# Optimization experiments

Hardware: AMD Instinct MI355X
Metric: run time of the kernel (lower is better)

## Reference

```python
import jax, jax.numpy as jnp
import numpy as np

NUM_EXPERTS = 16
TOP_K = 2
D_STATE = 32
INPUT_DIM = 512
COPIES = 4
B, H, W = 64, 32, 32
NOISE_KEY = jax.random.key(42)


def setup_inputs() -> dict:
    key = jax.random.key(0)
    k1, k2, k3 = jax.random.split(key, 3)
    inputs = jax.random.normal(k1, (B, INPUT_DIM, H, W), dtype=jnp.float32)
    W_route = jax.random.normal(k2, (INPUT_DIM, NUM_EXPERTS), dtype=jnp.float32) * 0.02
    b_route = jnp.zeros((NUM_EXPERTS,), dtype=jnp.float32)
    W_noise = jax.random.normal(k3, (INPUT_DIM, NUM_EXPERTS), dtype=jnp.float32) * 0.02
    b_noise = jnp.zeros((NUM_EXPERTS,), dtype=jnp.float32)
    # A_log_init: log(arange(1..d_state)) repeated over d_inner, copies, merged
    A = jnp.log(jnp.arange(1, D_STATE + 1, dtype=jnp.float32))            # [n]
    A = jnp.broadcast_to(A, (COPIES * INPUT_DIM, D_STATE))                # [copies*d, n]
    A_logs = jnp.broadcast_to(A, (NUM_EXPERTS, COPIES * INPUT_DIM, D_STATE)).copy()
    return {"inputs": inputs, "W_route": W_route, "b_route": b_route,
            "W_noise": W_noise, "b_noise": b_noise, "A_logs": A_logs}


def reference(inputs, W_route, b_route, W_noise, b_noise, A_logs):
    # Router: spatial mean pool -> [B, input_dim]
    x = inputs.mean(axis=(2, 3))
    logits = jax.nn.softmax(x @ W_route + b_route, axis=-1)               # [B, E]
    noise_logits = x @ W_noise + b_noise                                  # [B, E]
    eps = jax.random.normal(NOISE_KEY, logits.shape, dtype=logits.dtype)
    noise = jax.nn.softmax(eps * jax.nn.softplus(noise_logits), axis=-1)
    noisy_logits = logits + noise                                         # [B, E]
    top_k_logits, indices = jax.lax.top_k(noisy_logits, TOP_K)            # [B, k]
    router_output = jax.nn.softmax(top_k_logits, axis=-1)                 # [B, k]
    # Dispatch: gather selected expert A_log tables -> [B, k, copies*d, n]
    expert_outputs = A_logs[indices]
    # Weighted combine then mean over batch -> [copies*d, n]
    combined = jnp.einsum('bnik,bn->bik', expert_outputs, router_output).mean(axis=0)
    # z-loss over noisy logits
    z_loss = jnp.sum(jax.nn.logsumexp(noisy_logits, axis=-1) ** 2) / noisy_logits.shape[0]
    return combined, z_loss
```

## Files before the change

kernel.cpp:

```cpp
#include <hip/hip_runtime.h>
#include <hip/hip_bf16.h>
#include <math.h>
#include <stdint.h>


__global__ __launch_bounds__(256) void k_meanpool(const float* __restrict__ in,
                                                  float* __restrict__ x) {
  int gwave = (blockIdx.x * 256 + threadIdx.x) >> 6;
  int lane  = threadIdx.x & 63;
  const float4* p = reinterpret_cast<const float4*>(in) + (size_t)gwave * 256;
  float s = 0.f;
#pragma unroll
  for (int j = 0; j < 4; ++j) {
    float4 v = p[lane + 64 * j];
    s += (v.x + v.y) + (v.z + v.w);
  }
#pragma unroll
  for (int off = 32; off > 0; off >>= 1) s += __shfl_down(s, off, 64);
  if (lane == 0) x[gwave] = s * (1.0f / 1024.0f);
}

__device__ __forceinline__ uint32_t rotl32(uint32_t v, int d) {
  return (v << d) | (v >> (32 - d));
}

__device__ __forceinline__ void threefry2x32_0_42(uint32_t& x0, uint32_t& x1) {
  const uint32_t k0 = 0u, k1 = 42u;
  const uint32_t ks2 = k0 ^ k1 ^ 0x1BD11BDAu;
  x0 += k0; x1 += k1;
#define RND(rot) { x0 += x1; x1 = rotl32(x1, rot); x1 ^= x0; }
#define G4(a,b,c,d, ka,kb,inc) { RND(a) RND(b) RND(c) RND(d) x0 += ka; x1 += kb + inc; }
  G4(13,15,26,6,  k1,  ks2, 1u)
  G4(17,29,16,24, ks2, k0,  2u)
  G4(13,15,26,6,  k0,  k1,  3u)
  G4(17,29,16,24, k1,  ks2, 4u)
  G4(13,15,26,6,  ks2, k0,  5u)
#undef G4
#undef RND
}

__device__ __forceinline__ float erfinv_f32(float x) {
  float w = -log1pf(-x * x);
  float p;
  if (w < 5.0f) {
    w -= 2.5f;
    p = 2.81022636e-08f;
    p = fmaf(p, w, 3.43273939e-07f);
    p = fmaf(p, w, -3.5233877e-06f);
    p = fmaf(p, w, -4.39150654e-06f);
    p = fmaf(p, w, 0.00021858087f);
    p = fmaf(p, w, -0.00125372503f);
    p = fmaf(p, w, -0.00417768164f);
    p = fmaf(p, w, 0.246640727f);
    p = fmaf(p, w, 1.50140941f);
  } else {
    w = sqrtf(w) - 3.0f;
    p = -0.000200214257f;
    p = fmaf(p, w, 0.000100950558f);
    p = fmaf(p, w, 0.00134934322f);
    p = fmaf(p, w, -0.00367342844f);
    p = fmaf(p, w, 0.00573950773f);
    p = fmaf(p, w, -0.0076224613f);
    p = fmaf(p, w, 0.00943887047f);
    p = fmaf(p, w, 1.00167406f);
    p = fmaf(p, w, 2.83297682f);
  }
  return p * x;
}

__global__ __launch_bounds__(256) void k_router(
    const float* __restrict__ x,
    const float* __restrict__ Wr, const float* __restrict__ br,
    const float* __restrict__ Wn, const float* __restrict__ bn,
    int* __restrict__ idx, float* __restrict__ rw, float* __restrict__ lseArr) {
  __shared__ float xs[512];
  __shared__ float pr[16][17], pn[16][17];
  __shared__ float lg[16], nl[16], npre[16], noisy[16];
  const int b = blockIdx.x, tid = threadIdx.x;

  for (int d = tid; d < 512; d += 256) xs[d] = x[b * 512 + d];
  __syncthreads();

  const int e = tid & 15, c = tid >> 4;
  float sr = 0.f, sn = 0.f;
#pragma unroll 8
  for (int j = 0; j < 32; ++j) {
    int d = c * 32 + j;
    float xv = xs[d];
    sr = fmaf(xv, Wr[d * 16 + e], sr);
    sn = fmaf(xv, Wn[d * 16 + e], sn);
  }
  pr[c][e] = sr;
  pn[c][e] = sn;
  __syncthreads();

  if (tid < 16) {
    float a = 0.f, bb = 0.f;
    for (int cc = 0; cc < 16; ++cc) { a += pr[cc][tid]; bb += pn[cc][tid]; }
    lg[tid] = a + br[tid];
    float v = bb + bn[tid];
    nl[tid] = v;
    uint32_t i  = (uint32_t)(b * 16 + tid);
    uint32_t j  = i & 511u;
    uint32_t x0 = j, x1 = j + 512u;
    threefry2x32_0_42(x0, x1);
    uint32_t bits = (i < 512u) ? x0 : x1;
    float u01 = __uint_as_float((bits >> 9) | 0x3f800000u) - 1.0f;
    const float lo = -0.99999994f;
    float u = fmaf(u01, 1.0f - lo, lo);
    u = fmaxf(lo, u);
    float eps = 1.41421356f * erfinv_f32(u);
    float sp = fmaxf(v, 0.f) + log1pf(expf(-fabsf(v)));
    npre[tid] = eps * sp;
  }
  __syncthreads();

  if (tid < 16) {
    float ml = -INFINITY, mn = -INFINITY;
    for (int q = 0; q < 16; ++q) { ml = fmaxf(ml, lg[q]); mn = fmaxf(mn, npre[q]); }
    float sl = 0.f, sn2 = 0.f;
    for (int q = 0; q < 16; ++q) { sl += expf(lg[q] - ml); sn2 += expf(npre[q] - mn); }
    noisy[tid] = expf(lg[tid] - ml) / sl + expf(npre[tid] - mn) / sn2;
  }
  __syncthreads();

  if (tid == 0) {
    int i0 = 0; float v0 = noisy[0];
    for (int q = 1; q < 16; ++q) if (noisy[q] > v0) { v0 = noisy[q]; i0 = q; }
    int i1 = -1; float v1 = -INFINITY;
    for (int q = 0; q < 16; ++q) {
      if (q == i0) continue;
      if (noisy[q] > v1) { v1 = noisy[q]; i1 = q; }
    }
    float t = expf(v1 - v0);
    float inv = 1.0f / (1.0f + t);
    idx[b * 2 + 0] = i0; idx[b * 2 + 1] = i1;
    rw [b * 2 + 0] = inv; rw [b * 2 + 1] = t * inv;
    float m = -INFINITY;
    for (int q = 0; q < 16; ++q) m = fmaxf(m, noisy[q]);
    float s2 = 0.f;
    for (int q = 0; q < 16; ++q) s2 += expf(noisy[q] - m);
    lseArr[b] = m + logf(s2);
  }
}

__global__ __launch_bounds__(64) void k_reduce(const int* __restrict__ idx,
                                               const float* __restrict__ rw,
                                               const float* __restrict__ lse,
                                               float* __restrict__ w,
                                               float* __restrict__ zout) {
  int tid = threadIdx.x;
  if (tid < 16) {
    float acc = 0.f;
    for (int j = 0; j < 128; ++j)
      if (idx[j] == tid) acc += rw[j];
    w[tid] = acc * (1.0f / 64.0f);
  }
  if (tid == 32) {
    float z = 0.f;
    for (int b = 0; b < 64; ++b) { float l = lse[b]; z += l * l; }
    zout[0] = z * (1.0f / 64.0f);
  }
}

__global__ __launch_bounds__(256) void k_combine(const float* __restrict__ A,
                                                 const float* __restrict__ w,
                                                 float* __restrict__ out) {
  int t = blockIdx.x * 256 + threadIdx.x;
  const float4* A4 = reinterpret_cast<const float4*>(A);
  float4 acc = make_float4(0.f, 0.f, 0.f, 0.f);
#pragma unroll
  for (int e = 0; e < 16; ++e) {
    float we = w[e];
    float4 v = A4[e * 16384 + t];
    acc.x = fmaf(we, v.x, acc.x);
    acc.y = fmaf(we, v.y, acc.y);
    acc.z = fmaf(we, v.z, acc.z);
    acc.w = fmaf(we, v.w, acc.w);
  }
  reinterpret_cast<float4*>(out)[t] = acc;
}

extern "C" void kernel_launch(void* const* d_in, const int* in_sizes, int n_in,
                              void* d_out, int out_size, void* d_ws, size_t ws_size,
                              hipStream_t stream) {
  const float* inputs = (const float*)d_in[0];
  const float* Wr     = (const float*)d_in[1];
  const float* br     = (const float*)d_in[2];
  const float* Wn     = (const float*)d_in[3];
  const float* bn     = (const float*)d_in[4];
  const float* A      = (const float*)d_in[5];
  float* out = (float*)d_out;

  char* ws   = (char*)d_ws;
  float* x   = (float*)(ws);
  int*   idx = (int*)  (ws + 131072);
  float* rw  = (float*)(ws + 131584);
  float* lse = (float*)(ws + 132096);
  float* w   = (float*)(ws + 132352);

  hipLaunchKernelGGL(k_meanpool, dim3(8192), dim3(256), 0, stream, inputs, x);
  hipLaunchKernelGGL(k_router,   dim3(64),   dim3(256), 0, stream, x, Wr, br, Wn, bn, idx, rw, lse);
  hipLaunchKernelGGL(k_reduce,   dim3(1),    dim3(64),  0, stream, idx, rw, lse, w, out + 65536);
  hipLaunchKernelGGL(k_combine,  dim3(64),   dim3(256), 0, stream, A, w, out);
}
```

Baseline: 226.6 us.

## Fuse router, reduce and combine into one kernel with grid-level flag sync

Merges the router, expert-weight reduction and combine kernels into a single 64-block kernel. The last block to arrive, identified through an atomic ticket counter, computes the expert weights and z-loss, then releases a flag that the other blocks spin on before they run the combine. The counter and flag are reset inside the mean-pool kernel, and the mean-pool input reads become nontemporal loads. This removes two kernel launches and their gaps, in exchange for a spin-wait that relies on all 64 blocks being resident at the same time.

```diff
diff --git a/kernel.cpp b/kernel.cpp
--- a/kernel.cpp
+++ b/kernel.cpp
@@ -4,15 +4,22 @@
 #include <stdint.h>
 
 
+#define AGENT __HIP_MEMORY_SCOPE_AGENT
+
+typedef float fvec4 __attribute__((ext_vector_type(4)));
+
 __global__ __launch_bounds__(256) void k_meanpool(const float* __restrict__ in,
-                                                  float* __restrict__ x) {
+                                                  float* __restrict__ x,
+                                                  unsigned int* __restrict__ counter,
+                                                  unsigned int* __restrict__ flag) {
+  if (blockIdx.x == 0 && threadIdx.x == 0) { *counter = 0u; *flag = 0u; }
   int gwave = (blockIdx.x * 256 + threadIdx.x) >> 6;
   int lane  = threadIdx.x & 63;
-  const float4* p = reinterpret_cast<const float4*>(in) + (size_t)gwave * 256;
+  const fvec4* p = reinterpret_cast<const fvec4*>(in) + (size_t)gwave * 256;
   float s = 0.f;
 #pragma unroll
   for (int j = 0; j < 4; ++j) {
-    float4 v = p[lane + 64 * j];
+    fvec4 v = __builtin_nontemporal_load(&p[lane + 64 * j]);
     s += (v.x + v.y) + (v.z + v.w);
   }
 #pragma unroll
@@ -68,14 +75,19 @@
   return p * x;
 }
 
-__global__ __launch_bounds__(256) void k_router(
+__global__ __launch_bounds__(256) void k_tail(
     const float* __restrict__ x,
     const float* __restrict__ Wr, const float* __restrict__ br,
     const float* __restrict__ Wn, const float* __restrict__ bn,
-    int* __restrict__ idx, float* __restrict__ rw, float* __restrict__ lseArr) {
+    const float* __restrict__ A,
+    float* __restrict__ out,
+    int* __restrict__ idx, float* __restrict__ rw, float* __restrict__ lseArr,
+    float* __restrict__ w,
+    unsigned int* __restrict__ counter, unsigned int* __restrict__ flag) {
   __shared__ float xs[512];
   __shared__ float pr[16][17], pn[16][17];
-  __shared__ float lg[16], nl[16], npre[16], noisy[16];
+  __shared__ float lg[16], npre[16], noisy[16];
+  __shared__ unsigned int sTicket;
   const int b = blockIdx.x, tid = threadIdx.x;
 
   for (int d = tid; d < 512; d += 256) xs[d] = x[b * 512 + d];
@@ -99,7 +111,6 @@
     for (int cc = 0; cc < 16; ++cc) { a += pr[cc][tid]; bb += pn[cc][tid]; }
     lg[tid] = a + br[tid];
     float v = bb + bn[tid];
-    nl[tid] = v;
     uint32_t i  = (uint32_t)(b * 16 + tid);
     uint32_t j  = i & 511u;
     uint32_t x0 = j, x1 = j + 512u;
@@ -134,45 +145,63 @@
     }
     float t = expf(v1 - v0);
     float inv = 1.0f / (1.0f + t);
-    idx[b * 2 + 0] = i0; idx[b * 2 + 1] = i1;
-    rw [b * 2 + 0] = inv; rw [b * 2 + 1] = t * inv;
+    __hip_atomic_store(&idx[b * 2 + 0], i0,      __ATOMIC_RELAXED, AGENT);
+    __hip_atomic_store(&idx[b * 2 + 1], i1,      __ATOMIC_RELAXED, AGENT);
+    __hip_atomic_store(&rw [b * 2 + 0], inv,     __ATOMIC_RELAXED, AGENT);
+    __hip_atomic_store(&rw [b * 2 + 1], t * inv, __ATOMIC_RELAXED, AGENT);
     float m = -INFINITY;
     for (int q = 0; q < 16; ++q) m = fmaxf(m, noisy[q]);
     float s2 = 0.f;
     for (int q = 0; q < 16; ++q) s2 += expf(noisy[q] - m);
-    lseArr[b] = m + logf(s2);
-  }
-}
-
-__global__ __launch_bounds__(64) void k_reduce(const int* __restrict__ idx,
-                                               const float* __restrict__ rw,
-                                               const float* __restrict__ lse,
-                                               float* __restrict__ w,
-                                               float* __restrict__ zout) {
-  int tid = threadIdx.x;
-  if (tid < 16) {
-    float acc = 0.f;
-    for (int j = 0; j < 128; ++j)
-      if (idx[j] == tid) acc += rw[j];
-    w[tid] = acc * (1.0f / 64.0f);
-  }
-  if (tid == 32) {
-    float z = 0.f;
-    for (int b = 0; b < 64; ++b) { float l = lse[b]; z += l * l; }
-    zout[0] = z * (1.0f / 64.0f);
-  }
-}
-
-__global__ __launch_bounds__(256) void k_combine(const float* __restrict__ A,
-                                                 const float* __restrict__ w,
-                                                 float* __restrict__ out) {
-  int t = blockIdx.x * 256 + threadIdx.x;
+    __hip_atomic_store(&lseArr[b], m + logf(s2), __ATOMIC_RELAXED, AGENT);
+    __threadfence();
+    sTicket = atomicAdd(counter, 1u);
+  }
+  __syncthreads();
+
+  if (sTicket == 63u) {
+    __threadfence();
+    if (tid < 16) {
+      float acc = 0.f;
+      for (int j = 0; j < 128; ++j) {
+        int ij = __hip_atomic_load(&idx[j], __ATOMIC_RELAXED, AGENT);
+        if (ij == tid) acc += __hip_atomic_load(&rw[j], __ATOMIC_RELAXED, AGENT);
+      }
+      __hip_atomic_store(&w[tid], acc * (1.0f / 64.0f), __ATOMIC_RELAXED, AGENT);
+    }
+    if (tid == 32) {
+      float z = 0.f;
+      for (int bb = 0; bb < 64; ++bb) {
+        float l = __hip_atomic_load(&lseArr[bb], __ATOMIC_RELAXED, AGENT);
+        z += l * l;
+      }
+      out[65536] = z * (1.0f / 64.0f);
+    }
+    __syncthreads();
+    if (tid == 0) {
+      __threadfence();
+      __hip_atomic_store(flag, 1u, __ATOMIC_RELEASE, AGENT);
+    }
+  } else {
+    if (tid == 0) {
+      while (__hip_atomic_load(flag, __ATOMIC_ACQUIRE, AGENT) != 1u)
+        __builtin_amdgcn_s_sleep(2);
+    }
+    __syncthreads();
+  }
+
+  float wl[16];
+#pragma unroll
+  for (int q = 0; q < 16; ++q)
+    wl[q] = __hip_atomic_load(&w[q], __ATOMIC_RELAXED, AGENT);
+
+  int t = b * 256 + tid;
   const float4* A4 = reinterpret_cast<const float4*>(A);
   float4 acc = make_float4(0.f, 0.f, 0.f, 0.f);
 #pragma unroll
-  for (int e = 0; e < 16; ++e) {
-    float we = w[e];
-    float4 v = A4[e * 16384 + t];
+  for (int q = 0; q < 16; ++q) {
+    float we = wl[q];
+    float4 v = A4[q * 16384 + t];
     acc.x = fmaf(we, v.x, acc.x);
     acc.y = fmaf(we, v.y, acc.y);
     acc.z = fmaf(we, v.z, acc.z);
@@ -198,9 +227,11 @@
   float* rw  = (float*)(ws + 131584);
   float* lse = (float*)(ws + 132096);
   float* w   = (float*)(ws + 132352);
-
-  hipLaunchKernelGGL(k_meanpool, dim3(8192), dim3(256), 0, stream, inputs, x);
-  hipLaunchKernelGGL(k_router,   dim3(64),   dim3(256), 0, stream, x, Wr, br, Wn, bn, idx, rw, lse);
-  hipLaunchKernelGGL(k_reduce,   dim3(1),    dim3(64),  0, stream, idx, rw, lse, w, out + 65536);
-  hipLaunchKernelGGL(k_combine,  dim3(64),   dim3(256), 0, stream, A, w, out);
-}
+  unsigned int* counter = (unsigned int*)(ws + 132416);
+  unsigned int* flag    = (unsigned int*)(ws + 132420);
+
+  hipLaunchKernelGGL(k_meanpool, dim3(8192), dim3(256), 0, stream,
+                     inputs, x, counter, flag);
+  hipLaunchKernelGGL(k_tail, dim3(64), dim3(256), 0, stream,
+                     x, Wr, br, Wn, bn, A, out, idx, rw, lse, w, counter, flag);
+}
```

Result: slower. 265.2 us (+17.0%).
